# Optimization experiments

Hardware: AMD Instinct MI355X
Metric: run time of the kernel (lower is better)

## Reference

```python
import jax, jax.numpy as jnp
import numpy as np

B, T, F = 256, 192, 8
CARD0, CARD1 = 1000, 100
E0, E1 = 32, 16
H = 512
D_IN = F + E0 + E1  # 56


def _glorot(key, shape):
    fan_in, fan_out = shape[0], shape[-1]
    lim = jnp.sqrt(6.0 / (fan_in + fan_out))
    return jax.random.uniform(key, shape, jnp.float32, -lim, lim)


def setup_inputs() -> dict:
    key = jax.random.key(0)
    ks = jax.random.split(key, 16)
    return {
        "x_cont": jax.random.normal(ks[0], (B, T, F), jnp.float32),
        "cat0": jax.random.randint(ks[1], (B, T), 0, CARD0),
        "cat1": jax.random.randint(ks[2], (B, T), 0, CARD1),
        "emb0": _glorot(ks[3], (CARD0, E0)),
        "emb1": _glorot(ks[4], (CARD1, E1)),
        "Wk1": _glorot(ks[5], (D_IN, 4 * H)),
        "Wr1": _glorot(ks[6], (H, 4 * H)),
        "b1": jnp.zeros((4 * H,), jnp.float32).at[H:2 * H].set(1.0),  # unit_forget_bias
        "Wk2": _glorot(ks[7], (H, 4 * H)),
        "Wr2": _glorot(ks[8], (H, 4 * H)),
        "b2": jnp.zeros((4 * H,), jnp.float32).at[H:2 * H].set(1.0),
        "Wmu": _glorot(ks[9], (H, 1)),
        "bmu": _glorot(ks[10], (1, 1))[0],
        "Wsig": _glorot(ks[11], (H, 1)),
        "bsig": _glorot(ks[12], (1, 1))[0],
    }


def _lstm(x, Wk, Wr, b):
    # x: [B, T, D]; Keras gate order i, f, g(c), o; zero initial states (inference mode,
    # dropout/recurrent_dropout inactive when training=False).
    xz = jnp.einsum('btd,dk->btk', x, Wk) + b  # precompute input projection for all steps
    h0 = jnp.zeros((x.shape[0], H), x.dtype)

    def step(carry, z_t):
        h, c = carry
        z = z_t + h @ Wr  # [B, 4H]
        i, f, g, o = jnp.split(z, 4, axis=-1)
        i = jax.nn.sigmoid(i)
        f = jax.nn.sigmoid(f)
        g = jnp.tanh(g)
        o = jax.nn.sigmoid(o)
        c = f * c + i * g
        h = o * jnp.tanh(c)
        return (h, c), h

    _, hs = jax.lax.scan(step, (h0, h0), jnp.swapaxes(xz, 0, 1))  # [T, B, H]
    return jnp.swapaxes(hs, 0, 1)


def reference(x_cont, cat0, cat1, emb0, emb1, Wk1, Wr1, b1, Wk2, Wr2, b2, Wmu, bmu, Wsig, bsig):
    x = jnp.concatenate([x_cont, emb0[cat0], emb1[cat1]], axis=-1)  # [B, T, 56]
    x = _lstm(x, Wk1, Wr1, b1)
    x = _lstm(x, Wk2, Wr2, b2)
    mu = x @ Wmu + bmu                      # count_data=False -> raw mu
    sigma = jax.nn.softplus(x @ Wsig + bsig)
    return (mu, sigma)
```

## Files before the change

### kernel.cpp

```cpp
#include <hip/hip_runtime.h>
#include <math.h>

#define Bsz 256
#define Tsz 192
#define Fc 8
#define E0c 32
#define E1c 16
#define Hc 512
#define G4 2048
#define DINP 64
#define K1t 576
#define K2t 1024
#define NBLK 256
#define LBLK 32
#define KPAD1 584
#define KPAD2 1032
#define LDSB_BYTES (64 * KPAD2 * 2)
#define SLOT_STRIDE 16

typedef __attribute__((ext_vector_type(8))) short short8;
typedef __attribute__((ext_vector_type(4))) float f32x4;

static __device__ __forceinline__ float bf2f(ushort u) {
    return __uint_as_float(((uint)u) << 16);
}
static __device__ __forceinline__ ushort f2bf(float f) {
    uint u = __float_as_uint(f);
    u = (u + 0x7fffu + ((u >> 16) & 1u)) >> 16;
    return (ushort)u;
}

static __device__ __forceinline__ uint poll_sc1(const uint* p) {
    uint v;
    asm volatile("global_load_dword %0, %1, off sc1\n\t"
                 "s_waitcnt vmcnt(0)"
                 : "=v"(v) : "v"((unsigned long long)p) : "memory");
    return v;
}
static __device__ __forceinline__ void store_slot_sc1(uint* p, uint v) {
    asm volatile("global_store_dword %0, %1, off sc1"
                 :: "v"((unsigned long long)p), "v"(v) : "memory");
}

__global__ __launch_bounds__(256) void build_x_kernel(
    const float* __restrict__ x_cont, const int* __restrict__ cat0,
    const int* __restrict__ cat1, const float* __restrict__ emb0,
    const float* __restrict__ emb1, ushort* __restrict__ x_bf)
{
    int idx = blockIdx.x * 256 + threadIdx.x;
    if (idx >= Tsz * Bsz * DINP) return;
    int d = idx & 63;
    int row = idx >> 6;
    int t = row >> 8;
    int b = row & 255;
    float v = 0.f;
    if (d < Fc)                  v = x_cont[(b * Tsz + t) * Fc + d];
    else if (d < Fc + E0c)       v = emb0[cat0[b * Tsz + t] * E0c + (d - Fc)];
    else if (d < Fc + E0c + E1c) v = emb1[cat1[b * Tsz + t] * E1c + (d - Fc - E0c)];
    x_bf[idx] = f2bf(v);
}

__global__ __launch_bounds__(256) void transpose_w_kernel(
    const float* __restrict__ in, ushort* __restrict__ out, int K, int ldout, int coff)
{
    __shared__ float tile[32][33];
    int k0 = blockIdx.x * 32;
    int n0 = blockIdx.y * 32;
    int tx = threadIdx.x & 31, ty = threadIdx.x >> 5;
    #pragma unroll
    for (int p = 0; p < 4; ++p) {
        int k = k0 + ty + p * 8;
        tile[ty + p * 8][tx] = (k < K) ? in[k * G4 + n0 + tx] : 0.f;
    }
    __syncthreads();
    #pragma unroll
    for (int p = 0; p < 4; ++p) {
        int nl = ty + p * 8;
        out[(size_t)(n0 + nl) * ldout + coff + k0 + tx] = f2bf(tile[tx][nl]);
    }
}

static __device__ __forceinline__ void wait2(const uint* a, uint ta, const uint* b, uint tb) {
    int tid = threadIdx.x;
    if (tid < 64) {
        const uint* p = (tid < 32) ? (a + (tid & 31) * SLOT_STRIDE)
                                   : (b + (tid & 31) * SLOT_STRIDE);
        uint tg = (tid < 32) ? ta : tb;
        while (true) {
            uint v = poll_sc1(p);
            if (__all((int)(v >= tg))) break;
            __builtin_amdgcn_s_sleep(1);
        }
    }
    __syncthreads();
}

template<int KS_IN, int KS_TOT, int LDA_IN, int KPADv>
static __device__ __forceinline__ void run_layer(
    const ushort* __restrict__ Ain,
    ushort* __restrict__ hbuf,
    const ushort* __restrict__ hz,
    const ushort* __restrict__ Wt,
    const float* __restrict__ bias,
    ushort* B_lds,
    const uint* dep_slots, uint dep_off,
    uint* own_slots, uint* my_slot,
    int m0, int j0)
{
    constexpr int KL = KS_TOT * 32;
    constexpr int SEGS = KL / 8;
    int tid = threadIdx.x;
    int lane = tid & 63, wv = tid >> 6;
    int lane15 = lane & 15, quad = lane >> 4;

    for (int i = tid; i < 64 * SEGS; i += 256) {
        int row = i / SEGS, seg = i - row * SEGS;
        int gz = (row >> 4) * Hc + j0 + (row & 15);
        *(uint4*)&B_lds[row * KPADv + seg * 8] =
            *(const uint4*)(Wt + (size_t)gz * KL + seg * 8);
    }
    __syncthreads();

    float bgate[4];
    #pragma unroll
    for (int gt = 0; gt < 4; ++gt) bgate[gt] = bias[gt * Hc + j0 + lane15];
    float cst[4] = {0.f, 0.f, 0.f, 0.f};

    int arow = m0 + wv * 16 + lane15;
    int crow0 = m0 + wv * 16 + quad * 4;

    for (int t = 0; t < Tsz; ++t) {
        wait2(dep_slots, (uint)t + dep_off, own_slots, (uint)t);

        const ushort* A0 = Ain + (size_t)t * Bsz * LDA_IN;
        const ushort* A1 = (t > 0) ? (hbuf + (size_t)(t - 1) * Bsz * Hc) : hz;

        uint4 areg[KS_TOT];
        {
            const ushort* p0 = A0 + (size_t)arow * LDA_IN + quad * 8;
            #pragma unroll
            for (int ks = 0; ks < KS_IN; ++ks)
                areg[ks] = *(const uint4*)(p0 + ks * 32);
            const ushort* p1 = A1 + (size_t)arow * Hc + quad * 8;
            #pragma unroll
            for (int ks = 0; ks < KS_TOT - KS_IN; ++ks)
                areg[KS_IN + ks] = *(const uint4*)(p1 + ks * 32);
        }
        asm volatile("" ::: "memory");

        f32x4 acc[4];
        #pragma unroll
        for (int gt = 0; gt < 4; ++gt) acc[gt] = (f32x4){0.f, 0.f, 0.f, 0.f};

        #pragma unroll
        for (int ks = 0; ks < KS_TOT; ++ks) {
            short8 av = __builtin_bit_cast(short8, areg[ks]);
            #pragma unroll
            for (int gt = 0; gt < 4; ++gt) {
                short8 bfr = *(const short8*)&B_lds[(gt * 16 + lane15) * KPADv + ks * 32 + quad * 8];
                acc[gt] = __builtin_amdgcn_mfma_f32_16x16x32_bf16(av, bfr, acc[gt], 0, 0, 0);
            }
        }

        uint hv[4];
        #pragma unroll
        for (int r = 0; r < 4; ++r) {
            float zi = acc[0][r] + bgate[0];
            float zf = acc[1][r] + bgate[1];
            float zg = acc[2][r] + bgate[2];
            float zo = acc[3][r] + bgate[3];
            float ig = 1.f / (1.f + __expf(-zi));
            float fg = 1.f / (1.f + __expf(-zf));
            float gg = tanhf(zg);
            float og = 1.f / (1.f + __expf(-zo));
            float cn = fg * cst[r] + ig * gg;
            cst[r] = cn;
            float hn = og * tanhf(cn);
            hv[r] = (uint)f2bf(hn);
        }
        {
            unsigned long long hb = (unsigned long long)
                &hbuf[((size_t)t * Bsz + crow0) * Hc + j0 + lane15];
            asm volatile(
                "global_store_short %0, %1, off sc1\n\t"
                "global_store_short %0, %2, off offset:1024 sc1\n\t"
                "global_store_short %0, %3, off offset:2048 sc1\n\t"
                "global_store_short %0, %4, off offset:3072 sc1\n\t"
                "s_waitcnt vmcnt(0)"
                :: "v"(hb), "v"(hv[0]), "v"(hv[1]), "v"(hv[2]), "v"(hv[3])
                : "memory");
        }

        __syncthreads();
        if (tid == 0)
            store_slot_sc1(my_slot, (uint)(t + 1));
    }
}

__global__ __launch_bounds__(256, 1) void deepar_persistent(
    const ushort* __restrict__ x_bf,
    const ushort* __restrict__ Wt1, const ushort* __restrict__ Wt2,
    const float* __restrict__ b1, const float* __restrict__ b2,
    ushort* __restrict__ h1, ushort* __restrict__ h2,
    const ushort* __restrict__ hz,
    const float* __restrict__ Wmu, const float* __restrict__ bmu,
    const float* __restrict__ Wsig, const float* __restrict__ bsig,
    float* __restrict__ out, uint* __restrict__ slots)
{
    extern __shared__ ushort B_lds[];

    int bid = blockIdx.x;
    int xcd = bid & 7;
    int g = xcd >> 1;
    int role = xcd & 1;
    int jb = bid >> 3;
    int m0 = g * 64;
    int j0 = jb * 16;
    uint* s_l1 = slots + (g * 2 + 0) * LBLK * SLOT_STRIDE;
    uint* s_l2 = slots + (g * 2 + 1) * LBLK * SLOT_STRIDE;

    if (role == 0) {
        run_layer<2, 18, DINP, KPAD1>(x_bf, h1, hz, Wt1, b1, B_lds,
                                      s_l1, 0u, s_l1, s_l1 + jb * SLOT_STRIDE, m0, j0);
        return;
    }
    run_layer<16, 32, Hc, KPAD2>(h1, h2, hz, Wt2, b2, B_lds,
                                 s_l1, 1u, s_l2, s_l2 + jb * SLOT_STRIDE, m0, j0);

    wait2(s_l2, (uint)Tsz, s_l2, (uint)Tsz);

    int lane = threadIdx.x & 63, wv = threadIdx.x >> 6;
    float wm[8], wsg[8];
    #pragma unroll
    for (int i = 0; i < 8; ++i) {
        wm[i] = Wmu[lane * 8 + i];
        wsg[i] = Wsig[lane * 8 + i];
    }
    float bmu0 = bmu[0], bsg0 = bsig[0];
    for (int i = jb * 4 + wv; i < 64 * Tsz; i += 128) {
        int b = m0 + (i & 63);
        int t = i >> 6;
        const ushort* hp = h2 + ((size_t)t * Bsz + b) * Hc + lane * 8;
        short8 hvv = *(const short8*)hp;
        float smu = 0.f, ssg = 0.f;
        #pragma unroll
        for (int e = 0; e < 8; ++e) {
            float f = bf2f((ushort)hvv[e]);
            smu += f * wm[e];
            ssg += f * wsg[e];
        }
        #pragma unroll
        for (int off = 32; off > 0; off >>= 1) {
            smu += __shfl_down(smu, off, 64);
            ssg += __shfl_down(ssg, off, 64);
        }
        if (lane == 0) {
            int oi = b * Tsz + t;
            float sg = ssg + bsg0;
            float sp = sg > 0.f ? sg + log1pf(__expf(-sg)) : log1pf(__expf(sg));
            out[oi] = smu + bmu0;
            out[Bsz * Tsz + oi] = sp;
        }
    }
}

extern "C" void kernel_launch(void* const* d_in, const int* in_sizes, int n_in,
                              void* d_out, int out_size, void* d_ws, size_t ws_size,
                              hipStream_t stream) {
    const float* x_cont = (const float*)d_in[0];
    const int*   cat0   = (const int*)d_in[1];
    const int*   cat1   = (const int*)d_in[2];
    const float* emb0   = (const float*)d_in[3];
    const float* emb1   = (const float*)d_in[4];
    const float* Wk1    = (const float*)d_in[5];
    const float* Wr1    = (const float*)d_in[6];
    const float* b1     = (const float*)d_in[7];
    const float* Wk2    = (const float*)d_in[8];
    const float* Wr2    = (const float*)d_in[9];
    const float* b2     = (const float*)d_in[10];
    const float* Wmu    = (const float*)d_in[11];
    const float* bmu    = (const float*)d_in[12];
    const float* Wsig   = (const float*)d_in[13];
    const float* bsig   = (const float*)d_in[14];
    float* out = (float*)d_out;

    const size_t slots_bytes = 8 * LBLK * SLOT_STRIDE * 4;

    char* ws = (char*)d_ws;
    uint*   slots = (uint*)ws;                                 ws += slots_bytes;
    ushort* x_bf  = (ushort*)ws;                               ws += (size_t)Tsz * Bsz * DINP * 2;
    ushort* Wt1   = (ushort*)ws;                               ws += (size_t)G4 * K1t * 2;
    ushort* Wt2   = (ushort*)ws;                               ws += (size_t)G4 * K2t * 2;
    ushort* h1    = (ushort*)ws;                               ws += (size_t)Tsz * Bsz * Hc * 2;
    ushort* h2    = (ushort*)ws;                               ws += (size_t)Tsz * Bsz * Hc * 2;
    ushort* hz    = (ushort*)ws;                               ws += (size_t)Bsz * Hc * 2;

    hipMemsetAsync(slots, 0, slots_bytes, stream);
    hipMemsetAsync(hz, 0, (size_t)Bsz * Hc * 2, stream);

    build_x_kernel<<<(Tsz * Bsz * DINP + 255) / 256, 256, 0, stream>>>(
        x_cont, cat0, cat1, emb0, emb1, x_bf);
    transpose_w_kernel<<<dim3(2, 64), 256, 0, stream>>>(Wk1, Wt1, 56, K1t, 0);
    transpose_w_kernel<<<dim3(16, 64), 256, 0, stream>>>(Wr1, Wt1, Hc, K1t, DINP);
    transpose_w_kernel<<<dim3(16, 64), 256, 0, stream>>>(Wk2, Wt2, Hc, K2t, 0);
    transpose_w_kernel<<<dim3(16, 64), 256, 0, stream>>>(Wr2, Wt2, Hc, K2t, Hc);

    hipFuncSetAttribute((const void*)deepar_persistent,
                        hipFuncAttributeMaxDynamicSharedMemorySize, LDSB_BYTES);
    deepar_persistent<<<dim3(NBLK), dim3(256), LDSB_BYTES, stream>>>(
        x_bf, Wt1, Wt2, b1, b2, h1, h2, hz, Wmu, bmu, Wsig, bsig, out, slots);
}
```

Before: 1.429 ms.

## Split per-step wait so input-projection MFMAs overlap the recurrent-state barrier

Each timestep's combined wait on the dependency and own-layer slots is split in two. The input-projection part of the GEMM is computed first, after waiting only on the upstream layer; only then does the block wait for the recurrent h(t-1) from sibling blocks before the recurrent part. Layer 1 skips the dependency wait entirely, and the t=0 step skips the own-slot wait. The aim is to hide cross-block synchronisation latency behind useful MFMA work, at the cost of an extra __syncthreads per step and code restructured with static_for.

```diff
diff --git a/kernel.cpp b/kernel.cpp
--- a/kernel.cpp
+++ b/kernel.cpp
@@ -21,6 +21,15 @@
 typedef __attribute__((ext_vector_type(8))) short short8;
 typedef __attribute__((ext_vector_type(4))) float f32x4;
 
+template<int N> struct IC { static constexpr int v = N; };
+template<int C, int CMAX, typename F>
+__device__ __forceinline__ void static_for(F&& f) {
+    if constexpr (C < CMAX) {
+        f(IC<C>{});
+        static_for<C + 1, CMAX>(f);
+    }
+}
+
 static __device__ __forceinline__ float bf2f(ushort u) {
     return __uint_as_float(((uint)u) << 16);
 }
@@ -80,22 +89,16 @@
     }
 }
 
-static __device__ __forceinline__ void wait2(const uint* a, uint ta, const uint* b, uint tb) {
-    int tid = threadIdx.x;
-    if (tid < 64) {
-        const uint* p = (tid < 32) ? (a + (tid & 31) * SLOT_STRIDE)
-                                   : (b + (tid & 31) * SLOT_STRIDE);
-        uint tg = (tid < 32) ? ta : tb;
-        while (true) {
-            uint v = poll_sc1(p);
-            if (__all((int)(v >= tg))) break;
-            __builtin_amdgcn_s_sleep(1);
-        }
-    }
-    __syncthreads();
-}
-
-template<int KS_IN, int KS_TOT, int LDA_IN, int KPADv>
+static __device__ __forceinline__ void wait_slots(const uint* arr, uint tg) {
+    const uint* p = arr + (threadIdx.x & 31) * SLOT_STRIDE;
+    while (true) {
+        uint v = poll_sc1(p);
+        if (__all((int)(v >= tg))) break;
+        __builtin_amdgcn_s_sleep(1);
+    }
+}
+
+template<int KS_IN, int KS_TOT, int LDA_IN, int KPADv, bool HAS_DEP>
 static __device__ __forceinline__ void run_layer(
     const ushort* __restrict__ Ain,
     ushort* __restrict__ hbuf,
@@ -103,10 +106,11 @@
     const ushort* __restrict__ Wt,
     const float* __restrict__ bias,
     ushort* B_lds,
-    const uint* dep_slots, uint dep_off,
+    const uint* dep_slots,
     uint* own_slots, uint* my_slot,
     int m0, int j0)
 {
+    constexpr int KS_R = KS_TOT - KS_IN;
     constexpr int KL = KS_TOT * 32;
     constexpr int SEGS = KL / 8;
     int tid = threadIdx.x;
@@ -130,36 +134,55 @@
     int crow0 = m0 + wv * 16 + quad * 4;
 
     for (int t = 0; t < Tsz; ++t) {
-        wait2(dep_slots, (uint)t + dep_off, own_slots, (uint)t);
-
-        const ushort* A0 = Ain + (size_t)t * Bsz * LDA_IN;
-        const ushort* A1 = (t > 0) ? (hbuf + (size_t)(t - 1) * Bsz * Hc) : hz;
-
-        uint4 areg[KS_TOT];
-        {
-            const ushort* p0 = A0 + (size_t)arow * LDA_IN + quad * 8;
-            #pragma unroll
-            for (int ks = 0; ks < KS_IN; ++ks)
-                areg[ks] = *(const uint4*)(p0 + ks * 32);
-            const ushort* p1 = A1 + (size_t)arow * Hc + quad * 8;
-            #pragma unroll
-            for (int ks = 0; ks < KS_TOT - KS_IN; ++ks)
-                areg[KS_IN + ks] = *(const uint4*)(p1 + ks * 32);
-        }
-        asm volatile("" ::: "memory");
-
         f32x4 acc[4];
         #pragma unroll
         for (int gt = 0; gt < 4; ++gt) acc[gt] = (f32x4){0.f, 0.f, 0.f, 0.f};
 
-        #pragma unroll
-        for (int ks = 0; ks < KS_TOT; ++ks) {
-            short8 av = __builtin_bit_cast(short8, areg[ks]);
-            #pragma unroll
-            for (int gt = 0; gt < 4; ++gt) {
-                short8 bfr = *(const short8*)&B_lds[(gt * 16 + lane15) * KPADv + ks * 32 + quad * 8];
-                acc[gt] = __builtin_amdgcn_mfma_f32_16x16x32_bf16(av, bfr, acc[gt], 0, 0, 0);
-            }
+        if constexpr (HAS_DEP) {
+            if (tid < 64) wait_slots(dep_slots, (uint)(t + 1));
+            __syncthreads();
+        }
+        {
+            const ushort* p0 = Ain + ((size_t)t * Bsz + arow) * LDA_IN + quad * 8;
+            uint4 bufA[KS_IN];
+            static_for<0, KS_IN>([&](auto Kc) {
+                constexpr int ks = decltype(Kc)::v;
+                bufA[ks] = *(const uint4*)(p0 + ks * 32);
+            });
+            asm volatile("" ::: "memory");
+            static_for<0, KS_IN>([&](auto Kc) {
+                constexpr int ks = decltype(Kc)::v;
+                short8 av = __builtin_bit_cast(short8, bufA[ks]);
+                #pragma unroll
+                for (int gt = 0; gt < 4; ++gt) {
+                    short8 bfr = *(const short8*)&B_lds[(gt * 16 + lane15) * KPADv + ks * 32 + quad * 8];
+                    acc[gt] = __builtin_amdgcn_mfma_f32_16x16x32_bf16(av, bfr, acc[gt], 0, 0, 0);
+                }
+            });
+        }
+
+        if (t) {
+            if (tid < 64) wait_slots(own_slots, (uint)t);
+            __syncthreads();
+        }
+        {
+            const ushort* p1base = (t > 0) ? (hbuf + (size_t)(t - 1) * Bsz * Hc) : hz;
+            const ushort* p1 = p1base + (size_t)arow * Hc + quad * 8;
+            uint4 bufB[KS_R];
+            static_for<0, KS_R>([&](auto Kc) {
+                constexpr int ks = decltype(Kc)::v;
+                bufB[ks] = *(const uint4*)(p1 + ks * 32);
+            });
+            asm volatile("" ::: "memory");
+            static_for<0, KS_R>([&](auto Kc) {
+                constexpr int ks = decltype(Kc)::v;
+                short8 av = __builtin_bit_cast(short8, bufB[ks]);
+                #pragma unroll
+                for (int gt = 0; gt < 4; ++gt) {
+                    short8 bfr = *(const short8*)&B_lds[(gt * 16 + lane15) * KPADv + (KS_IN + ks) * 32 + quad * 8];
+                    acc[gt] = __builtin_amdgcn_mfma_f32_16x16x32_bf16(av, bfr, acc[gt], 0, 0, 0);
+                }
+            });
         }
 
         uint hv[4];
@@ -220,14 +243,15 @@
     uint* s_l2 = slots + (g * 2 + 1) * LBLK * SLOT_STRIDE;
 
     if (role == 0) {
-        run_layer<2, 18, DINP, KPAD1>(x_bf, h1, hz, Wt1, b1, B_lds,
-                                      s_l1, 0u, s_l1, s_l1 + jb * SLOT_STRIDE, m0, j0);
+        run_layer<2, 18, DINP, KPAD1, false>(x_bf, h1, hz, Wt1, b1, B_lds,
+                                             nullptr, s_l1, s_l1 + jb * SLOT_STRIDE, m0, j0);
         return;
     }
-    run_layer<16, 32, Hc, KPAD2>(h1, h2, hz, Wt2, b2, B_lds,
-                                 s_l1, 1u, s_l2, s_l2 + jb * SLOT_STRIDE, m0, j0);
-
-    wait2(s_l2, (uint)Tsz, s_l2, (uint)Tsz);
+    run_layer<16, 32, Hc, KPAD2, true>(h1, h2, hz, Wt2, b2, B_lds,
+                                       s_l1, s_l2, s_l2 + jb * SLOT_STRIDE, m0, j0);
+
+    if (threadIdx.x < 64) wait_slots(s_l2, (uint)Tsz);
+    __syncthreads();
 
     int lane = threadIdx.x & 63, wv = threadIdx.x >> 6;
     float wm[8], wsg[8];
```

After: 1.364 ms. 1.05x faster.
